# Kernel optimization log

Hardware: AMD Instinct MI355X
Metric: run time of the kernel (lower is better)

The kernel has to match this reference:

```python
import jax, jax.numpy as jnp
from jax import lax
import numpy as np

KS = 3          # kernel_size
PAD = 1         # padding of conv_offset
N = KS * KS     # sampling points per pixel
B, C, H, W = 8, 64, 96, 96
OUTC = 64


def setup_inputs() -> dict:
    key = jax.random.key(0)
    k1, k2, k3 = jax.random.split(key, 3)
    x = jax.random.normal(k1, (B, C, H, W), dtype=jnp.float32)
    # conv_offset: Conv2d(C, 2N, ks=3, pad=1); small init so offsets are modest
    w_off = jax.random.normal(k2, (2 * N, C, KS, KS), dtype=jnp.float32) * 0.01
    b_off = jnp.zeros((2 * N,), jnp.float32)
    # conv_kernel: Conv2d(C, OUTC, ks=3, stride=3)
    w_ker = jax.random.normal(k3, (OUTC, C, KS, KS), dtype=jnp.float32) * (1.0 / np.sqrt(C * KS * KS))
    b_ker = jnp.zeros((OUTC,), jnp.float32)
    return {"x": x, "w_off": w_off, "b_off": b_off, "w_ker": w_ker, "b_ker": b_ker}


def _deform_conv(x, w_off, b_off, w_ker, b_ker):
    b, c, h, w = x.shape
    dn = ('NCHW', 'OIHW', 'NCHW')
    # offset field: (b, 2N, h, w); channels [:N] are x(row) offsets, [N:] are y(col)
    offset = lax.conv_general_dilated(x, w_off, (1, 1), [(PAD, PAD), (PAD, PAD)],
                                      dimension_numbers=dn) + b_off[None, :, None, None]
    r = jnp.arange(-(KS - 1) // 2, (KS - 1) // 2 + 1)
    pnx, pny = jnp.meshgrid(r, r, indexing='ij')          # kernel grid offsets p_n
    gx, gy = jnp.meshgrid(jnp.arange(h), jnp.arange(w), indexing='ij')  # p_0
    px = gx[None, None].astype(x.dtype) + pnx.reshape(1, N, 1, 1).astype(x.dtype) + offset[:, :N]
    py = gy[None, None].astype(x.dtype) + pny.reshape(1, N, 1, 1).astype(x.dtype) + offset[:, N:]
    # Bilinear sampling with zero outside the grid. This is exactly the dense
    # G @ x of the original (only the 4 neighbors of p have nonzero G weight).
    x0 = jnp.floor(px); y0 = jnp.floor(py)
    lx = px - x0; ly = py - y0            # grads flow to offsets through lx/ly
    x0i = lax.stop_gradient(x0).astype(jnp.int32)
    y0i = lax.stop_gradient(y0).astype(jnp.int32)
    x_flat = x.transpose(0, 2, 3, 1).reshape(b, h * w, c)  # (b, HW, c)

    def corner(xi, yi, wt):
        valid = ((xi >= 0) & (xi < h) & (yi >= 0) & (yi < w)).astype(x.dtype)
        idx = (jnp.clip(xi, 0, h - 1) * w + jnp.clip(yi, 0, w - 1)).reshape(b, -1)
        g = jax.vmap(lambda im, ix: im[ix])(x_flat, idx)   # (b, N*h*w, c)
        return g * (wt * valid).reshape(b, -1, 1)

    val = (corner(x0i,     y0i,     (1 - lx) * (1 - ly))
           + corner(x0i + 1, y0i,     lx * (1 - ly))
           + corner(x0i,     y0i + 1, (1 - lx) * ly)
           + corner(x0i + 1, y0i + 1, lx * ly))            # (b, N*h*w, c)
    xo = val.reshape(b, N, h, w, c).transpose(0, 4, 2, 3, 1)        # (b,c,h,w,N)
    # _reshape_x_offset: N -> (kr,kc) tiled into (h*ks, w*ks)
    xo = xo.reshape(b, c, h, w, KS, KS).transpose(0, 1, 2, 4, 3, 5).reshape(b, c, h * KS, w * KS)
    out = lax.conv_general_dilated(xo, w_ker, (KS, KS), 'VALID',
                                   dimension_numbers=dn) + b_ker[None, :, None, None]
    return out  # (b, OUTC, h, w)


def reference(x, w_off, b_off, w_ker, b_ker):
    return _deform_conv(x, w_off, b_off, w_ker, b_ker)
```

## Files before the change

### kernel.cpp

```cpp
#include <hip/hip_runtime.h>

#define H_ 96
#define W_ 96
#define HW 9216
#define C_ 64
#define OUTC 64
#define NPTS 9
#define NCH 18
#define B_ 8
#define NPIX 73728

#define PCH 72

typedef __attribute__((ext_vector_type(8))) short short8;
typedef __attribute__((ext_vector_type(4))) float f32x4;
typedef __attribute__((ext_vector_type(4))) unsigned int uint4v;

__device__ __forceinline__ short f2bf(float f) {
    union { float f; unsigned u; } v; v.f = f;
    unsigned r = v.u + 0x7fffu + ((v.u >> 16) & 1u);
    return (short)(r >> 16);
}
__device__ __forceinline__ float bflo(unsigned d) {
    union { unsigned u; float f; } v; v.u = d << 16; return v.f;
}
__device__ __forceinline__ float bfhi(unsigned d) {
    union { unsigned u; float f; } v; v.u = d & 0xffff0000u; return v.f;
}

__global__ __launch_bounds__(256) void prep_xpose(
    const float* __restrict__ x, const float* __restrict__ w_ker,
    const float* __restrict__ w_off, short* __restrict__ x_t,
    short* __restrict__ wk_frag, short* __restrict__ woff_frag)
{
    int blk = blockIdx.x;
    int t   = threadIdx.x;
    if (blk < 1152) {
        int b   = blk & 7;
        int sub = blk >> 3;
        int cb  = t & 7;
        int pix = (sub * 32 + (t >> 3)) * 2;

        const float* xp = x + ((size_t)(b * C_ + cb * 8) * HW) + pix;
        float tl[8][2];
#pragma unroll
        for (int e = 0; e < 8; ++e) {
            float2 v = *(const float2*)(xp + (size_t)e * HW);
            tl[e][0] = v.x; tl[e][1] = v.y;
        }
#pragma unroll
        for (int p = 0; p < 2; ++p) {
            short8 s;
#pragma unroll
            for (int e = 0; e < 8; ++e) s[e] = f2bf(tl[e][p]);
            *(short8*)(x_t + ((size_t)(b * HW + pix + p) * 64) + cb * 8) = s;
        }
    } else {
        int idx = (blk - 1152) * 256 + t;
        if (idx < 36864) {
            int j = idx & 7, l = (idx >> 3) & 63, nt = (idx >> 9) & 3, sg = idx >> 11;
            int q2 = sg & 1, n = sg >> 1;
            int c  = q2 * 32 + ((l >> 4) << 3) + j;
            int oc = nt * 16 + (l & 15);
            wk_frag[idx] = f2bf(w_ker[(oc * C_ + c) * 9 + n]);
        } else {
            int k = idx - 36864;
            int j = k & 7, l = (k >> 3) & 63, nt = (k >> 9) & 1, sg = k >> 10;
            int q2 = sg & 1, n = sg >> 1;
            int c  = q2 * 32 + ((l >> 4) << 3) + j;
            int oc = nt * 16 + (l & 15);
            woff_frag[k] = (oc < NCH) ? f2bf(w_off[(oc * C_ + c) * 9 + n]) : (short)0;
        }
    }
}

__global__ __launch_bounds__(256, 6) void deform_fused(
    const short* __restrict__ x_t, const short* __restrict__ woff_frag,
    const float* __restrict__ b_off, const short* __restrict__ wk_frag,
    const float* __restrict__ b_ker, float* __restrict__ out)
{
    __shared__ __align__(16) short sX[100 * PCH];
    __shared__ float  sE[64 * 20];
    __shared__ float2 sP[16 * 9];

    int t    = threadIdx.x;
    int lane = t & 63;
    int wv   = t >> 6;
    int b    = blockIdx.x & 7;
    int strip= blockIdx.x >> 3;
    int px0  = strip * 16;
    int i    = px0 / W_;
    int j0   = px0 - i * W_;
    int pxl  = lane & 15, kq = lane >> 4;
    int j    = j0 + pxl;
    const short* xb = x_t + (size_t)b * HW * 64;
    const short8 Z8 = {0,0,0,0,0,0,0,0};

    for (int u = t; u < 800; u += 256) {
        int cb = u & 7, rc = u >> 3;
        int r = rc / 20, c = rc - r * 20;
        int row = min(max(i - 2 + r, 0), H_ - 1);
        int col = min(max(j0 - 2 + c, 0), W_ - 1);
        *(short8*)&sX[rc * PCH + cb * 8] =
            *(const short8*)(xb + (row * W_ + col) * 64 + cb * 8);
    }
    __syncthreads();

    f32x4 pa0 = {0,0,0,0}, pa1 = {0,0,0,0};
    auto p1tap = [&](int n) {
        int di = n / 3 - 1, dj = n % 3 - 1;
        int ii = i + di, jj = j + dj;
        bool ok = (ii >= 0) & (ii < H_) & (jj >= 0) & (jj < W_);
        int rc = (di + 2) * 20 + (pxl + dj + 2);
#pragma unroll
        for (int q2 = 0; q2 < 2; ++q2) {
            short8 a = *(const short8*)&sX[rc * PCH + q2 * 32 + kq * 8];
            a = ok ? a : Z8;
            const short* wb = woff_frag + ((n * 2 + q2) * 2) * 512 + lane * 8;
            short8 b0 = *(const short8*)(wb);
            short8 b1 = *(const short8*)(wb + 512);
            pa0 = __builtin_amdgcn_mfma_f32_16x16x32_bf16(a, b0, pa0, 0, 0, 0);
            pa1 = __builtin_amdgcn_mfma_f32_16x16x32_bf16(a, b1, pa1, 0, 0, 0);
        }
    };
    if      (wv == 0) { p1tap(0); p1tap(1); }
    else if (wv == 1) { p1tap(2); p1tap(3); }
    else if (wv == 2) { p1tap(4); p1tap(5); }
    else              { p1tap(6); p1tap(7); p1tap(8); }
    {
        int col = lane & 15, rq = lane >> 4;
#pragma unroll
        for (int r = 0; r < 4; ++r)
            sE[(wv * 16 + rq * 4 + r) * 20 + col] = pa0[r];
        if (col < 2) {
#pragma unroll
            for (int r = 0; r < 4; ++r)
                sE[(wv * 16 + rq * 4 + r) * 20 + 16 + col] = pa1[r];
        }
    }
    __syncthreads();

    if (t < 144) {
        int p = t / 9, n = t - p * 9;
        float ox = sE[p * 20 + n]             + sE[(16 + p) * 20 + n]
                 + sE[(32 + p) * 20 + n]      + sE[(48 + p) * 20 + n]      + b_off[n];
        float oy = sE[p * 20 + 9 + n]         + sE[(16 + p) * 20 + 9 + n]
                 + sE[(32 + p) * 20 + 9 + n]  + sE[(48 + p) * 20 + 9 + n]  + b_off[9 + n];
        sP[p * 9 + n] = make_float2(ox, oy);
    }
    __syncthreads();

    f32x4 acc[4];
#pragma unroll
    for (int nt = 0; nt < 4; ++nt) acc[nt] = (f32x4){0.f, 0.f, 0.f, 0.f};

    auto p2tap = [&](int n) {
        int di = n / 3 - 1, dj = n % 3 - 1;
        float2 o = sP[pxl * 9 + n];
        float fpx = (float)(i + di) + o.x;
        float fpy = (float)(j + dj) + o.y;
        float x0f = floorf(fpx), y0f = floorf(fpy);
        float lx = fpx - x0f, ly = fpy - y0f;
        int xi = (int)x0f, yi = (int)y0f;
        float wx0 = (xi >= 0  && xi <= H_ - 1) ? (1.0f - lx) : 0.0f;
        float wx1 = (xi >= -1 && xi <= H_ - 2) ? lx          : 0.0f;
        float wy0 = (yi >= 0  && yi <= W_ - 1) ? (1.0f - ly) : 0.0f;
        float wy1 = (yi >= -1 && yi <= W_ - 2) ? ly          : 0.0f;
        float w00 = wx0 * wy0, w10 = wx1 * wy0, w01 = wx0 * wy1, w11 = wx1 * wy1;
        int rp = xi - (i - 2), cp = yi - (j0 - 2);
        bool inp = (rp >= 0) & (rp <= 3) & (cp >= 0) & (cp <= 18);
        uint4v u[8];
        if (inp) {
            int l00 = (rp * 20 + cp) * PCH;
            int l10 = l00 + 20 * PCH, l01 = l00 + PCH, l11 = l10 + PCH;
#pragma unroll
            for (int q2 = 0; q2 < 2; ++q2) {
                int cho = q2 * 32 + kq * 8;
                u[q2*4+0] = *(const uint4v*)&sX[l00 + cho];
                u[q2*4+1] = *(const uint4v*)&sX[l10 + cho];
                u[q2*4+2] = *(const uint4v*)&sX[l01 + cho];
                u[q2*4+3] = *(const uint4v*)&sX[l11 + cho];
            }
        }
        if (!inp) {
            int r0 = min(max(xi,     0), H_ - 1) * W_;
            int r1 = min(max(xi + 1, 0), H_ - 1) * W_;
            int c0 = min(max(yi,     0), W_ - 1);
            int c1 = min(max(yi + 1, 0), W_ - 1);
#pragma unroll
            for (int q2 = 0; q2 < 2; ++q2) {
                int cho = q2 * 32 + kq * 8;
                u[q2*4+0] = *(const uint4v*)(xb + (r0 + c0) * 64 + cho);
                u[q2*4+1] = *(const uint4v*)(xb + (r1 + c0) * 64 + cho);
                u[q2*4+2] = *(const uint4v*)(xb + (r0 + c1) * 64 + cho);
                u[q2*4+3] = *(const uint4v*)(xb + (r1 + c1) * 64 + cho);
            }
        }
#pragma unroll
        for (int q2 = 0; q2 < 2; ++q2) {
            short8 A;
#pragma unroll
            for (int d = 0; d < 4; ++d) {
                float lo = w00 * bflo(u[q2*4+0][d]) + w10 * bflo(u[q2*4+1][d])
                         + w01 * bflo(u[q2*4+2][d]) + w11 * bflo(u[q2*4+3][d]);
                float hi = w00 * bfhi(u[q2*4+0][d]) + w10 * bfhi(u[q2*4+1][d])
                         + w01 * bfhi(u[q2*4+2][d]) + w11 * bfhi(u[q2*4+3][d]);
                A[2 * d]     = f2bf(lo);
                A[2 * d + 1] = f2bf(hi);
            }
            const short* wbp = wk_frag + ((n * 2 + q2) * 4) * 512 + lane * 8;
#pragma unroll
            for (int nt = 0; nt < 4; ++nt) {
                short8 bfr = *(const short8*)(wbp + nt * 512);
                acc[nt] = __builtin_amdgcn_mfma_f32_16x16x32_bf16(A, bfr, acc[nt], 0, 0, 0);
            }
        }
    };
    if      (wv == 0) { p2tap(0); p2tap(1); }
    else if (wv == 1) { p2tap(2); p2tap(3); }
    else if (wv == 2) { p2tap(4); p2tap(5); }
    else              { p2tap(6); p2tap(7); p2tap(8); }

    __syncthreads();
    int col = lane & 15, rq = lane >> 4;
    if (wv == 0) {
#pragma unroll
        for (int nt = 0; nt < 4; ++nt) {
            int oc = nt * 16 + col;
            float bias = b_ker[oc];
#pragma unroll
            for (int r = 0; r < 4; ++r)
                sE[oc * 20 + rq * 4 + r] = acc[nt][r] + bias;
        }
    }
    __syncthreads();
    if (wv == 1) {
#pragma unroll
        for (int nt = 0; nt < 4; ++nt) {
            int oc = nt * 16 + col;
#pragma unroll
            for (int r = 0; r < 4; ++r)
                sE[oc * 20 + rq * 4 + r] += acc[nt][r];
        }
    }
    __syncthreads();
    if (wv == 2) {
#pragma unroll
        for (int nt = 0; nt < 4; ++nt) {
            int oc = nt * 16 + col;
#pragma unroll
            for (int r = 0; r < 4; ++r)
                sE[oc * 20 + rq * 4 + r] += acc[nt][r];
        }
    }
    __syncthreads();
    if (wv == 3) {
#pragma unroll
        for (int nt = 0; nt < 4; ++nt) {
            int oc = nt * 16 + col;
#pragma unroll
            for (int r = 0; r < 4; ++r)
                sE[oc * 20 + rq * 4 + r] += acc[nt][r];
        }
    }
    __syncthreads();

    int oc = t >> 2, qr = t & 3;
    const float* se = &sE[oc * 20 + qr * 4];
    float* outp = out + ((size_t)(b * OUTC + oc) * HW) + px0 + qr * 4;
    *(f32x4*)outp = *(const f32x4*)se;

}

extern "C" void kernel_launch(void* const* d_in, const int* in_sizes, int n_in,
                              void* d_out, int out_size, void* d_ws, size_t ws_size,
                              hipStream_t stream) {
    const float* x     = (const float*)d_in[0];
    const float* w_off = (const float*)d_in[1];
    const float* b_off = (const float*)d_in[2];
    const float* w_ker = (const float*)d_in[3];
    const float* b_ker = (const float*)d_in[4];
    float* out = (float*)d_out;

    char*  wsb       = (char*)d_ws;
    short* x_t       = (short*)wsb;
    short* wk_frag   = (short*)(wsb + 9437184);
    short* woff_frag = wk_frag + 36864;

    prep_xpose  <<<1368, 256, 0, stream>>>(x, w_ker, w_off, x_t, wk_frag, woff_frag);
    deform_fused<<<4608, 256, 0, stream>>>(x_t, woff_frag, b_off, wk_frag, b_ker, out);
}
```

Measured before the change: 111.4 us.

## Precompute bilinear weights per tap, parallel epilogue reduction, wider prep transpose

The prep transpose now has each thread convert 4 pixels with float4 loads, so half as many blocks are launched. In the fused kernel, the 144 offset threads now also compute the bilinear corner weights and pack the index and validity metadata into shared memory, so sampling waves no longer repeat that work. The serialized four-stage accumulation across waves is replaced by one shared-memory staging area per wave and a single parallel reduction, removing three barriers. Shared memory is aliased into one buffer, the occupancy hint is raised to 7, and the interpolation uses fma chains; the risk is register pressure at 7 waves per SIMD.

```diff
diff --git a/kernel.cpp b/kernel.cpp
--- a/kernel.cpp
+++ b/kernel.cpp
@@ -27,6 +27,12 @@
 __device__ __forceinline__ float bfhi(unsigned d) {
     union { unsigned u; float f; } v; v.u = d & 0xffff0000u; return v.f;
 }
+__device__ __forceinline__ float2 ub2(unsigned d) {
+    return make_float2(bflo(d), bfhi(d));
+}
+__device__ __forceinline__ float2 fma2(float s, float2 a, float2 b) {
+    return make_float2(fmaf(s, a.x, b.x), fmaf(s, a.y, b.y));
+}
 
 __global__ __launch_bounds__(256) void prep_xpose(
     const float* __restrict__ x, const float* __restrict__ w_ker,
@@ -35,28 +41,25 @@
 {
     int blk = blockIdx.x;
     int t   = threadIdx.x;
-    if (blk < 1152) {
+    if (blk < 576) {
         int b   = blk & 7;
         int sub = blk >> 3;
         int cb  = t & 7;
-        int pix = (sub * 32 + (t >> 3)) * 2;
-
-        const float* xp = x + ((size_t)(b * C_ + cb * 8) * HW) + pix;
-        float tl[8][2];
-#pragma unroll
-        for (int e = 0; e < 8; ++e) {
-            float2 v = *(const float2*)(xp + (size_t)e * HW);
-            tl[e][0] = v.x; tl[e][1] = v.y;
-        }
-#pragma unroll
-        for (int p = 0; p < 2; ++p) {
+        int px  = sub * 128 + (t >> 3) * 4;
+
+        const float* xp = x + ((size_t)(b * C_ + cb * 8) * HW) + px;
+        f32x4 tl[8];
+#pragma unroll
+        for (int e = 0; e < 8; ++e) tl[e] = *(const f32x4*)(xp + (size_t)e * HW);
+#pragma unroll
+        for (int p = 0; p < 4; ++p) {
             short8 s;
 #pragma unroll
             for (int e = 0; e < 8; ++e) s[e] = f2bf(tl[e][p]);
-            *(short8*)(x_t + ((size_t)(b * HW + pix + p) * 64) + cb * 8) = s;
+            *(short8*)(x_t + ((size_t)(b * HW + px + p) * 64) + cb * 8) = s;
         }
     } else {
-        int idx = (blk - 1152) * 256 + t;
+        int idx = (blk - 576) * 256 + t;
         if (idx < 36864) {
             int j = idx & 7, l = (idx >> 3) & 63, nt = (idx >> 9) & 3, sg = idx >> 11;
             int q2 = sg & 1, n = sg >> 1;
@@ -74,14 +77,16 @@
     }
 }
 
-__global__ __launch_bounds__(256, 6) void deform_fused(
+__global__ __launch_bounds__(256, 7) void deform_fused(
     const short* __restrict__ x_t, const short* __restrict__ woff_frag,
     const float* __restrict__ b_off, const short* __restrict__ wk_frag,
     const float* __restrict__ b_ker, float* __restrict__ out)
 {
-    __shared__ __align__(16) short sX[100 * PCH];
-    __shared__ float  sE[64 * 20];
-    __shared__ float2 sP[16 * 9];
+    __shared__ __align__(16) char smem[22400];
+    short* sX = (short*)smem;
+    float* sE = (float*)(smem + 14400);
+    float* sP = (float*)(smem + 19520);
+    float* sR = (float*)smem;
 
     int t    = threadIdx.x;
     int lane = t & 63;
@@ -142,23 +147,13 @@
 
     if (t < 144) {
         int p = t / 9, n = t - p * 9;
-        float ox = sE[p * 20 + n]             + sE[(16 + p) * 20 + n]
-                 + sE[(32 + p) * 20 + n]      + sE[(48 + p) * 20 + n]      + b_off[n];
-        float oy = sE[p * 20 + 9 + n]         + sE[(16 + p) * 20 + 9 + n]
-                 + sE[(32 + p) * 20 + 9 + n]  + sE[(48 + p) * 20 + 9 + n]  + b_off[9 + n];
-        sP[p * 9 + n] = make_float2(ox, oy);
-    }
-    __syncthreads();
-
-    f32x4 acc[4];
-#pragma unroll
-    for (int nt = 0; nt < 4; ++nt) acc[nt] = (f32x4){0.f, 0.f, 0.f, 0.f};
-
-    auto p2tap = [&](int n) {
+        float ox = sE[p * 20 + n]            + sE[(16 + p) * 20 + n]
+                 + sE[(32 + p) * 20 + n]     + sE[(48 + p) * 20 + n]     + b_off[n];
+        float oy = sE[p * 20 + 9 + n]        + sE[(16 + p) * 20 + 9 + n]
+                 + sE[(32 + p) * 20 + 9 + n] + sE[(48 + p) * 20 + 9 + n] + b_off[9 + n];
         int di = n / 3 - 1, dj = n % 3 - 1;
-        float2 o = sP[pxl * 9 + n];
-        float fpx = (float)(i + di) + o.x;
-        float fpy = (float)(j + dj) + o.y;
+        float fpx = (float)(i + di) + ox;
+        float fpy = (float)(j0 + p + dj) + oy;
         float x0f = floorf(fpx), y0f = floorf(fpy);
         float lx = fpx - x0f, ly = fpy - y0f;
         int xi = (int)x0f, yi = (int)y0f;
@@ -166,12 +161,32 @@
         float wx1 = (xi >= -1 && xi <= H_ - 2) ? lx          : 0.0f;
         float wy0 = (yi >= 0  && yi <= W_ - 1) ? (1.0f - ly) : 0.0f;
         float wy1 = (yi >= -1 && yi <= W_ - 2) ? ly          : 0.0f;
-        float w00 = wx0 * wy0, w10 = wx1 * wy0, w01 = wx0 * wy1, w11 = wx1 * wy1;
         int rp = xi - (i - 2), cp = yi - (j0 - 2);
         bool inp = (rp >= 0) & (rp <= 3) & (cp >= 0) & (cp <= 18);
+        int rc  = inp ? (rp * 20 + cp) : 0;
+        int xic = min(max(xi, -3), 100) + 3;
+        int yic = min(max(yi, -3), 100) + 3;
+        unsigned meta = (unsigned)rc | ((unsigned)inp << 7)
+                      | ((unsigned)xic << 8) | ((unsigned)yic << 15);
+        float* pp = &sP[t * 5];
+        pp[0] = wx0 * wy0; pp[1] = wx1 * wy0; pp[2] = wx0 * wy1; pp[3] = wx1 * wy1;
+        pp[4] = __uint_as_float(meta);
+    }
+    __syncthreads();
+
+    f32x4 acc[4];
+#pragma unroll
+    for (int nt = 0; nt < 4; ++nt) acc[nt] = (f32x4){0.f, 0.f, 0.f, 0.f};
+
+    auto p2tap = [&](int n) {
+        const float* pp = &sP[(pxl * 9 + n) * 5];
+        float w00 = pp[0], w10 = pp[1], w01 = pp[2], w11 = pp[3];
+        unsigned m = __float_as_uint(pp[4]);
+        int rc  = m & 0x7f;
+        bool inp = (m >> 7) & 1;
         uint4v u[8];
         if (inp) {
-            int l00 = (rp * 20 + cp) * PCH;
+            int l00 = rc * PCH;
             int l10 = l00 + 20 * PCH, l01 = l00 + PCH, l11 = l10 + PCH;
 #pragma unroll
             for (int q2 = 0; q2 < 2; ++q2) {
@@ -183,6 +198,8 @@
             }
         }
         if (!inp) {
+            int xi = (int)((m >> 8)  & 0x7f) - 3;
+            int yi = (int)((m >> 15) & 0x7f) - 3;
             int r0 = min(max(xi,     0), H_ - 1) * W_;
             int r1 = min(max(xi + 1, 0), H_ - 1) * W_;
             int c0 = min(max(yi,     0), W_ - 1);
@@ -201,12 +218,12 @@
             short8 A;
 #pragma unroll
             for (int d = 0; d < 4; ++d) {
-                float lo = w00 * bflo(u[q2*4+0][d]) + w10 * bflo(u[q2*4+1][d])
-                         + w01 * bflo(u[q2*4+2][d]) + w11 * bflo(u[q2*4+3][d]);
-                float hi = w00 * bfhi(u[q2*4+0][d]) + w10 * bfhi(u[q2*4+1][d])
-                         + w01 * bfhi(u[q2*4+2][d]) + w11 * bfhi(u[q2*4+3][d]);
-                A[2 * d]     = f2bf(lo);
-                A[2 * d + 1] = f2bf(hi);
+                float2 v = make_float2(w00 * bflo(u[q2*4+0][d]), w00 * bfhi(u[q2*4+0][d]));
+                v = fma2(w10, ub2(u[q2*4+1][d]), v);
+                v = fma2(w01, ub2(u[q2*4+2][d]), v);
+                v = fma2(w11, ub2(u[q2*4+3][d]), v);
+                A[2 * d]     = f2bf(v.x);
+                A[2 * d + 1] = f2bf(v.y);
             }
             const short* wbp = wk_frag + ((n * 2 + q2) * 4) * 512 + lane * 8;
 #pragma unroll
@@ -222,54 +239,30 @@
     else              { p2tap(6); p2tap(7); p2tap(8); }
 
     __syncthreads();
-    int col = lane & 15, rq = lane >> 4;
-    if (wv == 0) {
+    {
+        float* reg = sR + wv * 1088;
+        int col = lane & 15, rq = lane >> 4;
 #pragma unroll
         for (int nt = 0; nt < 4; ++nt) {
             int oc = nt * 16 + col;
-            float bias = b_ker[oc];
 #pragma unroll
             for (int r = 0; r < 4; ++r)
-                sE[oc * 20 + rq * 4 + r] = acc[nt][r] + bias;
-        }
-    }
-    __syncthreads();
-    if (wv == 1) {
-#pragma unroll
-        for (int nt = 0; nt < 4; ++nt) {
-            int oc = nt * 16 + col;
-#pragma unroll
-            for (int r = 0; r < 4; ++r)
-                sE[oc * 20 + rq * 4 + r] += acc[nt][r];
-        }
-    }
-    __syncthreads();
-    if (wv == 2) {
-#pragma unroll
-        for (int nt = 0; nt < 4; ++nt) {
-            int oc = nt * 16 + col;
-#pragma unroll
-            for (int r = 0; r < 4; ++r)
-                sE[oc * 20 + rq * 4 + r] += acc[nt][r];
-        }
-    }
-    __syncthreads();
-    if (wv == 3) {
-#pragma unroll
-        for (int nt = 0; nt < 4; ++nt) {
-            int oc = nt * 16 + col;
-#pragma unroll
-            for (int r = 0; r < 4; ++r)
-                sE[oc * 20 + rq * 4 + r] += acc[nt][r];
-        }
-    }
-    __syncthreads();
-
-    int oc = t >> 2, qr = t & 3;
-    const float* se = &sE[oc * 20 + qr * 4];
-    float* outp = out + ((size_t)(b * OUTC + oc) * HW) + px0 + qr * 4;
-    *(f32x4*)outp = *(const f32x4*)se;
-
+                reg[(rq * 4 + r) * 68 + oc] = acc[nt][r];
+        }
+    }
+    __syncthreads();
+    {
+        int oc = t >> 2, qr = t & 3;
+        float bias = b_ker[oc];
+        f32x4 v;
+#pragma unroll
+        for (int e = 0; e < 4; ++e) {
+            int px = qr * 4 + e;
+            v[e] = sR[px * 68 + oc] + sR[1088 + px * 68 + oc]
+                 + sR[2176 + px * 68 + oc] + sR[3264 + px * 68 + oc] + bias;
+        }
+        *(f32x4*)(out + ((size_t)(b * OUTC + oc) * HW) + px0 + qr * 4) = v;
+    }
 }
 
 extern "C" void kernel_launch(void* const* d_in, const int* in_sizes, int n_in,
@@ -287,6 +280,6 @@
     short* wk_frag   = (short*)(wsb + 9437184);
     short* woff_frag = wk_frag + 36864;
 
-    prep_xpose  <<<1368, 256, 0, stream>>>(x, w_ker, w_off, x_t, wk_frag, woff_frag);
+    prep_xpose  <<<792,  256, 0, stream>>>(x, w_ker, w_off, x_t, wk_frag, woff_frag);
     deform_fused<<<4608, 256, 0, stream>>>(x_t, woff_frag, b_off, wk_frag, b_ker, out);
 }
```

After: 115.4 us. 3.6% more time.
